# Performance work log

Hardware: AMD Instinct MI355X
Metric: run time of the kernel (lower is better)

The kernel has to match this reference:

```python
import jax, jax.numpy as jnp
import numpy as np

V = 2_000_000
NNZ = 14_000_000
N_MESHES = 4


def setup_inputs() -> dict:
    key = jax.random.key(0)
    k1, k2, k3, k4, k5, k6 = jax.random.split(key, 6)
    verts = jax.random.normal(k1, (V, 3), dtype=jnp.float32)
    lap_vals = jax.random.normal(k2, (NNZ,), dtype=jnp.float32)
    lap_rows = jax.random.randint(k3, (NNZ,), 0, V, dtype=jnp.int32)
    lap_cols = jax.random.randint(k4, (NNZ,), 0, V, dtype=jnp.int32)
    verts_mesh_idx = jnp.sort(jax.random.randint(k5, (V,), 0, N_MESHES, dtype=jnp.int32))
    coefs = jax.random.uniform(k6, (V,), dtype=jnp.float32)
    return {"verts": verts, "lap_vals": lap_vals, "lap_rows": lap_rows,
            "lap_cols": lap_cols, "verts_mesh_idx": verts_mesh_idx, "coefs": coefs}


def reference(verts, lap_vals, lap_rows, lap_cols, verts_mesh_idx, coefs):
    # Sparse Laplacian (COO) x vertex coords: L.mm(verts_packed)  [V,3]
    Lx = jax.ops.segment_sum(lap_vals[:, None] * verts[lap_cols], lap_rows,
                             num_segments=V)
    # norm_w = 1/rowsum where rowsum > 0, else unchanged (torch.sparse.sum dim=1)
    row_sum = jax.ops.segment_sum(lap_vals, lap_rows, num_segments=V)
    norm_w = jnp.where(row_sum > 0, 1.0 / jnp.where(row_sum > 0, row_sum, 1.0),
                       row_sum)[:, None]
    # 'cot' branch: loss = L.mm(verts) * norm_w - verts, then per-row L2 norm
    res = Lx * norm_w - verts
    loss = jnp.sqrt(jnp.sum(res * res, axis=1))  # [V]
    # weights = 1 / num_verts_per_mesh gathered per packed vertex
    nvpm = jnp.bincount(verts_mesh_idx, length=N_MESHES)
    weights = 1.0 / nvpm[verts_mesh_idx].astype(jnp.float32)
    loss = loss * weights * coefs
    return jnp.sum(loss) / N_MESHES
```

## Files before the change

### kernel.cpp

```cpp
#include <hip/hip_runtime.h>


#define NB 1024
#define BMAX 2048
#define BROWS 2048

__global__ void hist_kernel(const int* __restrict__ rows, int nnz, int cpb,
                            int B, unsigned short* __restrict__ hist,
                            const float* __restrict__ verts, int V,
                            float4* __restrict__ verts4) {
    if (verts4) {
        int stride = gridDim.x * blockDim.x;
        for (int vtx = blockIdx.x * blockDim.x + threadIdx.x; vtx < V;
             vtx += stride) {
            verts4[vtx] = make_float4(verts[3 * vtx + 0], verts[3 * vtx + 1],
                                      verts[3 * vtx + 2], 0.f);
        }
    }
    __shared__ unsigned h[BMAX];
    for (int b = threadIdx.x; b < B; b += blockDim.x) h[b] = 0;
    __syncthreads();
    int k = blockIdx.x;
    int i0 = k * cpb;
    int i1 = min(i0 + cpb, nnz);
    for (int i = i0 + 4 * (int)threadIdx.x; i < i1; i += 4 * blockDim.x) {
        if (i + 3 < i1) {
            int4 r4 = *(const int4*)(rows + i);
            atomicAdd(&h[r4.x >> 11], 1u);
            atomicAdd(&h[r4.y >> 11], 1u);
            atomicAdd(&h[r4.z >> 11], 1u);
            atomicAdd(&h[r4.w >> 11], 1u);
        } else {
            for (int j = i; j < i1; ++j) atomicAdd(&h[rows[j] >> 11], 1u);
        }
    }
    __syncthreads();
    for (int b = threadIdx.x; b < B; b += blockDim.x)
        hist[(size_t)b * NB + k] = (unsigned short)h[b];
}

__global__ void scan_blocks_kernel(unsigned short* __restrict__ hist,
                                   unsigned* __restrict__ total) {
    int b = blockIdx.x;
    int t = threadIdx.x;
    int lane = t & 63, wave = t >> 6;
    unsigned short* hp = hist + (size_t)b * NB;
    ushort4 hv = ((const ushort4*)hp)[t];
    unsigned a0 = hv.x, a1 = hv.y, a2 = hv.z, a3 = hv.w;
    unsigned sum = a0 + a1 + a2 + a3;
    unsigned x = sum;
    for (int off = 1; off < 64; off <<= 1) {
        unsigned y = __shfl_up(x, off);
        if (lane >= off) x += y;
    }
    __shared__ unsigned wsum[4];
    if (lane == 63) wsum[wave] = x;
    __syncthreads();
    unsigned woff = 0;
    for (int w = 0; w < wave; ++w) woff += wsum[w];
    unsigned excl = woff + x - sum;
    ushort4 ov;
    ov.x = (unsigned short)excl;
    ov.y = (unsigned short)(excl + a0);
    ov.z = (unsigned short)(excl + a0 + a1);
    ov.w = (unsigned short)(excl + a0 + a1 + a2);
    ((ushort4*)hp)[t] = ov;
    if (t == 255) total[b] = woff + x;
}

__global__ void scan_buckets_kernel(const unsigned* __restrict__ total,
                                    unsigned* __restrict__ base, int B,
                                    const int* __restrict__ mesh_idx, int v,
                                    int* __restrict__ nvpm) {
    int t = threadIdx.x;
    if (t < 4) {
        auto lb = [&](int tgt) {
            int lo = 0, hi = v;
            while (lo < hi) {
                int mid = (lo + hi) >> 1;
                if (mesh_idx[mid] < tgt) lo = mid + 1; else hi = mid;
            }
            return lo;
        };
        nvpm[t] = lb(t + 1) - lb(t);
    }
    __shared__ unsigned buf0[1024], buf1[1024];
    unsigned x0 = (2 * t < B) ? total[2 * t] : 0u;
    unsigned x1 = (2 * t + 1 < B) ? total[2 * t + 1] : 0u;
    unsigned pair = x0 + x1;
    buf0[t] = pair;
    __syncthreads();
    unsigned* src = buf0;
    unsigned* dst = buf1;
    unsigned vv = pair;
    for (int off = 1; off < 1024; off <<= 1) {
        vv = src[t];
        if (t >= off) vv += src[t - off];
        dst[t] = vv;
        __syncthreads();
        unsigned* tmp = src; src = dst; dst = tmp;
    }
    unsigned excl = vv - pair;
    base[2 * t] = excl;
    base[2 * t + 1] = excl + x0;
    if (t == 1023) base[2048] = vv;
}

__global__ void scatter_kernel(const int* __restrict__ rows,
                               const int* __restrict__ cols,
                               const float* __restrict__ vals,
                               const unsigned short* __restrict__ hist,
                               const unsigned* __restrict__ base,
                               uint2* __restrict__ dst,
                               int nnz, int cpb, int B) {
    __shared__ unsigned cur[BMAX];
    int k = blockIdx.x;
    for (int b = threadIdx.x; b < B; b += blockDim.x)
        cur[b] = base[b] + hist[(size_t)b * NB + k];
    __syncthreads();
    int i0 = k * cpb;
    int i1 = min(i0 + cpb, nnz);
    for (int i = i0 + 4 * (int)threadIdx.x; i < i1; i += 4 * blockDim.x) {
        if (i + 3 < i1) {
            int4   r4 = *(const int4*)(rows + i);
            int4   c4 = *(const int4*)(cols + i);
            float4 v4 = *(const float4*)(vals + i);
            unsigned p0 = atomicAdd(&cur[r4.x >> 11], 1u);
            unsigned p1 = atomicAdd(&cur[r4.y >> 11], 1u);
            unsigned p2 = atomicAdd(&cur[r4.z >> 11], 1u);
            unsigned p3 = atomicAdd(&cur[r4.w >> 11], 1u);
            uint2 e0, e1, e2, e3;
            e0.x = ((unsigned)(r4.x & (BROWS - 1)) << 21) | (unsigned)c4.x;
            e0.y = __float_as_uint(v4.x);
            e1.x = ((unsigned)(r4.y & (BROWS - 1)) << 21) | (unsigned)c4.y;
            e1.y = __float_as_uint(v4.y);
            e2.x = ((unsigned)(r4.z & (BROWS - 1)) << 21) | (unsigned)c4.z;
            e2.y = __float_as_uint(v4.z);
            e3.x = ((unsigned)(r4.w & (BROWS - 1)) << 21) | (unsigned)c4.w;
            e3.y = __float_as_uint(v4.w);
            dst[p0] = e0;
            dst[p1] = e1;
            dst[p2] = e2;
            dst[p3] = e3;
        } else {
            for (int j = i; j < i1; ++j) {
                int r = rows[j];
                unsigned p = atomicAdd(&cur[r >> 11], 1u);
                uint2 e;
                e.x = ((unsigned)(r & (BROWS - 1)) << 21) | (unsigned)cols[j];
                e.y = __float_as_uint(vals[j]);
                dst[p] = e;
            }
        }
    }
}

template <bool V4>
__global__ void bucket_kernel(const uint2* __restrict__ entries,
                              const unsigned* __restrict__ base,
                              const float* __restrict__ verts,
                              const float4* __restrict__ verts4,
                              const float* __restrict__ coefs,
                              const int* __restrict__ mesh_idx,
                              const int* __restrict__ nvpm,
                              double* __restrict__ partial, int V) {
    __shared__ float ax[BROWS], ay[BROWS], az[BROWS], aw[BROWS];
    int b = blockIdx.x;
    for (int j = threadIdx.x; j < BROWS; j += blockDim.x) {
        ax[j] = 0.f; ay[j] = 0.f; az[j] = 0.f; aw[j] = 0.f;
    }
    __syncthreads();
    unsigned s0 = base[b], s1 = base[b + 1];

    auto accum = [&](unsigned ex, unsigned ey) {
        unsigned lr = ex >> 21;
        unsigned c = ex & 0x1FFFFFu;
        float v = __uint_as_float(ey);
        float x, y, z;
        if (V4) {
            float4 p = verts4[c];
            x = p.x; y = p.y; z = p.z;
        } else {
            x = verts[3 * c + 0];
            y = verts[3 * c + 1];
            z = verts[3 * c + 2];
        }
        atomicAdd(&ax[lr], v * x);
        atomicAdd(&ay[lr], v * y);
        atomicAdd(&az[lr], v * z);
        atomicAdd(&aw[lr], v);
    };

    unsigned sA = s0 + (s0 & 1u);
    if (threadIdx.x == 0 && (s0 & 1u) && s0 < s1) {
        uint2 e = entries[s0];
        accum(e.x, e.y);
    }
    for (unsigned i = sA + 2 * threadIdx.x; i + 1 < s1; i += 2 * blockDim.x) {
        uint4 e = *(const uint4*)(entries + i);
        accum(e.x, e.y);
        accum(e.z, e.w);
    }
    if (threadIdx.x == 1 && s1 > sA && ((s1 - sA) & 1u)) {
        uint2 e = entries[s1 - 1];
        accum(e.x, e.y);
    }
    __syncthreads();

    float inv0 = 1.0f / (float)nvpm[0];
    float inv1 = 1.0f / (float)nvpm[1];
    float inv2 = 1.0f / (float)nvpm[2];
    float inv3 = 1.0f / (float)nvpm[3];

    double acc = 0.0;
    int r0 = b << 11;
    for (int j = threadIdx.x; j < BROWS; j += blockDim.x) {
        int r = r0 + j;
        if (r < V) {
            float rs = aw[j];
            float nw = (rs > 0.0f) ? (1.0f / rs) : rs;
            float vx, vy, vz;
            if (V4) {
                float4 p = verts4[r];
                vx = p.x; vy = p.y; vz = p.z;
            } else {
                vx = verts[3 * r + 0];
                vy = verts[3 * r + 1];
                vz = verts[3 * r + 2];
            }
            float d0 = ax[j] * nw - vx;
            float d1 = ay[j] * nw - vy;
            float d2 = az[j] * nw - vz;
            float loss = sqrtf(d0 * d0 + d1 * d1 + d2 * d2);
            int m = mesh_idx[r];
            float w = (m == 0) ? inv0 : (m == 1) ? inv1 : (m == 2) ? inv2 : inv3;
            acc += (double)(loss * w * coefs[r]);
        }
    }

    __shared__ double sred[512];
    sred[threadIdx.x] = acc;
    __syncthreads();
    for (int s = blockDim.x / 2; s > 0; s >>= 1) {
        if (threadIdx.x < s) sred[threadIdx.x] += sred[threadIdx.x + s];
        __syncthreads();
    }
    if (threadIdx.x == 0) atomicAdd(partial, sred[0]);
}

__global__ void write_out_kernel(const double* __restrict__ partial,
                                 float* __restrict__ out) {
    if (threadIdx.x == 0 && blockIdx.x == 0)
        out[0] = (float)(partial[0] * 0.25);
}


__global__ void fb_mesh_counts_kernel(const int* __restrict__ mesh_idx, int v,
                                      int* __restrict__ nvpm) {
    int m = threadIdx.x;
    if (m >= 4) return;
    auto lb = [&](int t) {
        int lo = 0, hi = v;
        while (lo < hi) {
            int mid = (lo + hi) >> 1;
            if (mesh_idx[mid] < t) lo = mid + 1; else hi = mid;
        }
        return lo;
    };
    nvpm[m] = lb(m + 1) - lb(m);
}

__global__ void fb_scatter_kernel(const float* __restrict__ verts,
                                  const float* __restrict__ vals,
                                  const int* __restrict__ rows,
                                  const int* __restrict__ cols,
                                  float* __restrict__ acc, int nnz) {
    int i = blockIdx.x * blockDim.x + threadIdx.x;
    if (i >= nnz) return;
    int r = rows[i];
    int c = cols[i];
    float v = vals[i];
    float* p = acc + 4ll * r;
    atomicAdd(p + 0, v * verts[3 * c + 0]);
    atomicAdd(p + 1, v * verts[3 * c + 1]);
    atomicAdd(p + 2, v * verts[3 * c + 2]);
    atomicAdd(p + 3, v);
}

__global__ void fb_finalize_kernel(const float* __restrict__ verts,
                                   const float* __restrict__ coefs,
                                   const int* __restrict__ mesh_idx,
                                   const float4* __restrict__ acc,
                                   const int* __restrict__ nvpm,
                                   double* __restrict__ partial, int v) {
    float inv0 = 1.0f / (float)nvpm[0];
    float inv1 = 1.0f / (float)nvpm[1];
    float inv2 = 1.0f / (float)nvpm[2];
    float inv3 = 1.0f / (float)nvpm[3];
    double acc_sum = 0.0;
    for (int i = blockIdx.x * blockDim.x + threadIdx.x; i < v;
         i += gridDim.x * blockDim.x) {
        float4 a = acc[i];
        float rs = a.w;
        float nw = (rs > 0.0f) ? (1.0f / rs) : rs;
        float r0 = a.x * nw - verts[3 * i + 0];
        float r1 = a.y * nw - verts[3 * i + 1];
        float r2 = a.z * nw - verts[3 * i + 2];
        float loss = sqrtf(r0 * r0 + r1 * r1 + r2 * r2);
        int m = mesh_idx[i];
        float w = (m == 0) ? inv0 : (m == 1) ? inv1 : (m == 2) ? inv2 : inv3;
        acc_sum += (double)(loss * w * coefs[i]);
    }
    __shared__ double sred[256];
    sred[threadIdx.x] = acc_sum;
    __syncthreads();
    for (int s = blockDim.x / 2; s > 0; s >>= 1) {
        if (threadIdx.x < s) sred[threadIdx.x] += sred[threadIdx.x + s];
        __syncthreads();
    }
    if (threadIdx.x == 0) atomicAdd(partial, sred[0]);
}

extern "C" void kernel_launch(void* const* d_in, const int* in_sizes, int n_in,
                              void* d_out, int out_size, void* d_ws, size_t ws_size,
                              hipStream_t stream) {
    const float* verts    = (const float*)d_in[0];
    const float* lap_vals = (const float*)d_in[1];
    const int*   lap_rows = (const int*)d_in[2];
    const int*   lap_cols = (const int*)d_in[3];
    const int*   mesh_idx = (const int*)d_in[4];
    const float* coefs    = (const float*)d_in[5];
    float* out = (float*)d_out;

    const int V   = in_sizes[0] / 3;
    const int NNZ = in_sizes[1];
    const int B   = (V + BROWS - 1) / BROWS;
    int cpb = (NNZ + NB - 1) / NB;
    cpb = (cpb + 3) & ~3;

    char* ws = (char*)d_ws;
    double*         partial = (double*)(ws + 0);
    int*            nvpm    = (int*)(ws + 8);
    unsigned*       base    = (unsigned*)(ws + 64);
    unsigned*       total   = (unsigned*)(ws + 16384);
    unsigned short* hist    = (unsigned short*)(ws + 32768);
    uint2*          entries = (uint2*)(ws + 32768 + (size_t)BMAX * NB * 2);

    size_t sort_need = 32768 + (size_t)BMAX * NB * 2 + (size_t)NNZ * 8 + 64;
    size_t v4_off    = (32768 + (size_t)BMAX * NB * 2 + (size_t)NNZ * 8 + 15)
                       & ~(size_t)15;
    size_t v4_need   = v4_off + (size_t)16 * V + 64;
    float4* verts4   = (float4*)(ws + v4_off);

    (void)hipMemsetAsync(d_ws, 0, 64, stream);

    if (ws_size >= sort_need && B <= BMAX && V <= (1 << 21)) {
        bool v4 = ws_size >= v4_need;
        hist_kernel<<<NB, 256, 0, stream>>>(lap_rows, NNZ, cpb, B, hist,
                                            verts, V, v4 ? verts4 : nullptr);
        scan_blocks_kernel<<<B, 256, 0, stream>>>(hist, total);
        scan_buckets_kernel<<<1, 1024, 0, stream>>>(total, base, B,
                                                    mesh_idx, V, nvpm);
        scatter_kernel<<<NB, 256, 0, stream>>>(lap_rows, lap_cols, lap_vals,
                                               hist, base, entries, NNZ, cpb, B);
        if (v4)
            bucket_kernel<true><<<B, 512, 0, stream>>>(
                entries, base, verts, verts4, coefs, mesh_idx, nvpm, partial, V);
        else
            bucket_kernel<false><<<B, 512, 0, stream>>>(
                entries, base, verts, verts4, coefs, mesh_idx, nvpm, partial, V);
    } else {
        float* acc = (float*)(ws + 64);
        (void)hipMemsetAsync(ws + 64, 0, (size_t)16 * V, stream);
        fb_mesh_counts_kernel<<<1, 64, 0, stream>>>(mesh_idx, V, nvpm);
        fb_scatter_kernel<<<(NNZ + 255) / 256, 256, 0, stream>>>(
            verts, lap_vals, lap_rows, lap_cols, acc, NNZ);
        fb_finalize_kernel<<<2048, 256, 0, stream>>>(
            verts, coefs, mesh_idx, (const float4*)acc, nvpm, partial, V);
    }

    write_out_kernel<<<1, 64, 0, stream>>>(partial, out);
}
```

Baseline: 692.5 us.

## Re-sort bucket entries by column segment to localize vertex gathers

Adds a resort pass that reorders each row bucket's entries by column segment (128K-vertex ranges) into a second entries buffer. A new bucket kernel then walks the segments in order, so concurrent blocks tend to gather verts4 from similar address ranges and get better cache locality. The price is an extra read and write of all NNZ entries, one more kernel launch, and extra workspace. It also uses nontemporal loads for the streamed entries, mesh_idx and coefs.

```diff
diff --git a/kernel.cpp b/kernel.cpp
--- a/kernel.cpp
+++ b/kernel.cpp
@@ -4,6 +4,11 @@
 #define NB 1024
 #define BMAX 2048
 #define BROWS 2048
+#define SEG_SHIFT 17
+#define NSEG_MAX 16
+
+typedef unsigned int uintv4 __attribute__((ext_vector_type(4)));
+typedef unsigned int uintv2 __attribute__((ext_vector_type(2)));
 
 __global__ void hist_kernel(const int* __restrict__ rows, int nnz, int cpb,
                             int B, unsigned short* __restrict__ hist,
@@ -155,6 +160,106 @@
     }
 }
 
+__global__ void resort_kernel(const uint2* __restrict__ src,
+                              const unsigned* __restrict__ base,
+                              uint2* __restrict__ dst,
+                              unsigned* __restrict__ segoff, int nseg) {
+    int b = blockIdx.x;
+    unsigned s0 = base[b], s1 = base[b + 1];
+    __shared__ unsigned cnt[8][NSEG_MAX];
+    __shared__ unsigned cur[NSEG_MAX];
+    int wave = threadIdx.x >> 6;
+    for (int s = threadIdx.x; s < 8 * NSEG_MAX; s += blockDim.x)
+        ((unsigned*)cnt)[s] = 0;
+    __syncthreads();
+    for (unsigned i = s0 + threadIdx.x; i < s1; i += blockDim.x) {
+        unsigned ex = ((const unsigned*)(src + i))[0];
+        atomicAdd(&cnt[wave][(ex & 0x1FFFFFu) >> SEG_SHIFT], 1u);
+    }
+    __syncthreads();
+    if (threadIdx.x == 0) {
+        unsigned acc = s0;
+        for (int s = 0; s < nseg; ++s) {
+            unsigned c = 0;
+            for (int w = 0; w < 8; ++w) c += cnt[w][s];
+            cur[s] = acc;
+            segoff[b * 17 + s] = acc;
+            acc += c;
+        }
+        segoff[b * 17 + nseg] = acc;
+    }
+    __syncthreads();
+    for (unsigned i = s0 + threadIdx.x; i < s1; i += blockDim.x) {
+        uint2 e = src[i];
+        unsigned p = atomicAdd(&cur[(e.x & 0x1FFFFFu) >> SEG_SHIFT], 1u);
+        dst[p] = e;
+    }
+}
+
+__global__ void bucket_seg_kernel(const uint2* __restrict__ entries,
+                                  const unsigned* __restrict__ segoff,
+                                  const float4* __restrict__ verts4,
+                                  const float* __restrict__ coefs,
+                                  const int* __restrict__ mesh_idx,
+                                  const int* __restrict__ nvpm,
+                                  double* __restrict__ partial, int V,
+                                  int nseg) {
+    __shared__ float ax[BROWS], ay[BROWS], az[BROWS], aw[BROWS];
+    int b = blockIdx.x;
+    for (int j = threadIdx.x; j < BROWS; j += blockDim.x) {
+        ax[j] = 0.f; ay[j] = 0.f; az[j] = 0.f; aw[j] = 0.f;
+    }
+    __syncthreads();
+    for (int s = 0; s < nseg; ++s) {
+        unsigned r0 = segoff[b * 17 + s];
+        unsigned r1 = segoff[b * 17 + s + 1];
+        for (unsigned i = r0 + threadIdx.x; i < r1; i += blockDim.x) {
+            uintv2 e = __builtin_nontemporal_load((const uintv2*)(entries + i));
+            unsigned lr = e.x >> 21;
+            unsigned c  = e.x & 0x1FFFFFu;
+            float4 p = verts4[c];
+            float v = __uint_as_float(e.y);
+            atomicAdd(&ax[lr], v * p.x);
+            atomicAdd(&ay[lr], v * p.y);
+            atomicAdd(&az[lr], v * p.z);
+            atomicAdd(&aw[lr], v);
+        }
+    }
+    __syncthreads();
+
+    float inv0 = 1.0f / (float)nvpm[0];
+    float inv1 = 1.0f / (float)nvpm[1];
+    float inv2 = 1.0f / (float)nvpm[2];
+    float inv3 = 1.0f / (float)nvpm[3];
+
+    double acc = 0.0;
+    int r0 = b << 11;
+    for (int j = threadIdx.x; j < BROWS; j += blockDim.x) {
+        int r = r0 + j;
+        if (r < V) {
+            float rs = aw[j];
+            float nw = (rs > 0.0f) ? (1.0f / rs) : rs;
+            float4 p = verts4[r];
+            float d0 = ax[j] * nw - p.x;
+            float d1 = ay[j] * nw - p.y;
+            float d2 = az[j] * nw - p.z;
+            float loss = sqrtf(d0 * d0 + d1 * d1 + d2 * d2);
+            int m = __builtin_nontemporal_load(mesh_idx + r);
+            float w = (m == 0) ? inv0 : (m == 1) ? inv1 : (m == 2) ? inv2 : inv3;
+            acc += (double)(loss * w * __builtin_nontemporal_load(coefs + r));
+        }
+    }
+
+    __shared__ double sred[512];
+    sred[threadIdx.x] = acc;
+    __syncthreads();
+    for (int s = blockDim.x / 2; s > 0; s >>= 1) {
+        if (threadIdx.x < s) sred[threadIdx.x] += sred[threadIdx.x + s];
+        __syncthreads();
+    }
+    if (threadIdx.x == 0) atomicAdd(partial, sred[0]);
+}
+
 template <bool V4>
 __global__ void bucket_kernel(const uint2* __restrict__ entries,
                               const unsigned* __restrict__ base,
@@ -172,11 +277,7 @@
     __syncthreads();
     unsigned s0 = base[b], s1 = base[b + 1];
 
-    auto accum = [&](unsigned ex, unsigned ey) {
-        unsigned lr = ex >> 21;
-        unsigned c = ex & 0x1FFFFFu;
-        float v = __uint_as_float(ey);
-        float x, y, z;
+    auto gather3 = [&](unsigned c, float& x, float& y, float& z) {
         if (V4) {
             float4 p = verts4[c];
             x = p.x; y = p.y; z = p.z;
@@ -185,25 +286,21 @@
             y = verts[3 * c + 1];
             z = verts[3 * c + 2];
         }
+    };
+    auto atomics = [&](unsigned ex, unsigned ey, float x, float y, float z) {
+        unsigned lr = ex >> 21;
+        float v = __uint_as_float(ey);
         atomicAdd(&ax[lr], v * x);
         atomicAdd(&ay[lr], v * y);
         atomicAdd(&az[lr], v * z);
         atomicAdd(&aw[lr], v);
     };
 
-    unsigned sA = s0 + (s0 & 1u);
-    if (threadIdx.x == 0 && (s0 & 1u) && s0 < s1) {
-        uint2 e = entries[s0];
-        accum(e.x, e.y);
-    }
-    for (unsigned i = sA + 2 * threadIdx.x; i + 1 < s1; i += 2 * blockDim.x) {
-        uint4 e = *(const uint4*)(entries + i);
-        accum(e.x, e.y);
-        accum(e.z, e.w);
-    }
-    if (threadIdx.x == 1 && s1 > sA && ((s1 - sA) & 1u)) {
-        uint2 e = entries[s1 - 1];
-        accum(e.x, e.y);
+    for (unsigned i = s0 + threadIdx.x; i < s1; i += blockDim.x) {
+        uint2 e = entries[i];
+        float x, y, z;
+        gather3(e.x & 0x1FFFFFu, x, y, z);
+        atomics(e.x, e.y, x, y, z);
     }
     __syncthreads();
 
@@ -220,14 +317,7 @@
             float rs = aw[j];
             float nw = (rs > 0.0f) ? (1.0f / rs) : rs;
             float vx, vy, vz;
-            if (V4) {
-                float4 p = verts4[r];
-                vx = p.x; vy = p.y; vz = p.z;
-            } else {
-                vx = verts[3 * r + 0];
-                vy = verts[3 * r + 1];
-                vz = verts[3 * r + 2];
-            }
+            gather3((unsigned)r, vx, vy, vz);
             float d0 = ax[j] * nw - vx;
             float d1 = ay[j] * nw - vy;
             float d2 = az[j] * nw - vz;
@@ -335,27 +425,34 @@
     const int V   = in_sizes[0] / 3;
     const int NNZ = in_sizes[1];
     const int B   = (V + BROWS - 1) / BROWS;
+    const int nseg = (V + (1 << SEG_SHIFT) - 1) >> SEG_SHIFT;
     int cpb = (NNZ + NB - 1) / NB;
     cpb = (cpb + 3) & ~3;
 
     char* ws = (char*)d_ws;
-    double*         partial = (double*)(ws + 0);
-    int*            nvpm    = (int*)(ws + 8);
-    unsigned*       base    = (unsigned*)(ws + 64);
-    unsigned*       total   = (unsigned*)(ws + 16384);
-    unsigned short* hist    = (unsigned short*)(ws + 32768);
-    uint2*          entries = (uint2*)(ws + 32768 + (size_t)BMAX * NB * 2);
-
-    size_t sort_need = 32768 + (size_t)BMAX * NB * 2 + (size_t)NNZ * 8 + 64;
-    size_t v4_off    = (32768 + (size_t)BMAX * NB * 2 + (size_t)NNZ * 8 + 15)
-                       & ~(size_t)15;
-    size_t v4_need   = v4_off + (size_t)16 * V + 64;
-    float4* verts4   = (float4*)(ws + v4_off);
+    const size_t off_hist     = 262144;
+    const size_t off_entries  = off_hist + (size_t)BMAX * NB * 2;
+    const size_t off_entries2 = off_entries + (size_t)NNZ * 8;
+    double*         partial  = (double*)(ws + 0);
+    int*            nvpm     = (int*)(ws + 8);
+    unsigned*       base     = (unsigned*)(ws + 64);
+    unsigned*       total    = (unsigned*)(ws + 16384);
+    unsigned*       segoff   = (unsigned*)(ws + 32768);
+    unsigned short* hist     = (unsigned short*)(ws + off_hist);
+    uint2*          entries  = (uint2*)(ws + off_entries);
+    uint2*          entries2 = (uint2*)(ws + off_entries2);
+
+    size_t sort_need = off_entries2 + 64;
+    size_t v4_need   = off_entries2 + (size_t)16 * V + 64;
+    size_t seg_need  = off_entries2 + (size_t)NNZ * 8 + (size_t)16 * V + 64;
 
     (void)hipMemsetAsync(d_ws, 0, 64, stream);
 
     if (ws_size >= sort_need && B <= BMAX && V <= (1 << 21)) {
-        bool v4 = ws_size >= v4_need;
+        bool seg = (ws_size >= seg_need) && (nseg <= NSEG_MAX);
+        bool v4  = seg || (ws_size >= v4_need);
+        float4* verts4 = seg ? (float4*)(ws + off_entries2 + (size_t)NNZ * 8)
+                             : (float4*)(ws + off_entries2);
         hist_kernel<<<NB, 256, 0, stream>>>(lap_rows, NNZ, cpb, B, hist,
                                             verts, V, v4 ? verts4 : nullptr);
         scan_blocks_kernel<<<B, 256, 0, stream>>>(hist, total);
@@ -363,12 +460,19 @@
                                                     mesh_idx, V, nvpm);
         scatter_kernel<<<NB, 256, 0, stream>>>(lap_rows, lap_cols, lap_vals,
                                                hist, base, entries, NNZ, cpb, B);
-        if (v4)
+        if (seg) {
+            resort_kernel<<<B, 512, 0, stream>>>(entries, base, entries2,
+                                                 segoff, nseg);
+            bucket_seg_kernel<<<B, 512, 0, stream>>>(entries2, segoff, verts4,
+                                                     coefs, mesh_idx, nvpm,
+                                                     partial, V, nseg);
+        } else if (v4) {
             bucket_kernel<true><<<B, 512, 0, stream>>>(
                 entries, base, verts, verts4, coefs, mesh_idx, nvpm, partial, V);
-        else
+        } else {
             bucket_kernel<false><<<B, 512, 0, stream>>>(
                 entries, base, verts, verts4, coefs, mesh_idx, nvpm, partial, V);
+        }
     } else {
         float* acc = (float*)(ws + 64);
         (void)hipMemsetAsync(ws + 64, 0, (size_t)16 * V, stream);
```

New measurement: 755.7 us. 1.09x slower.

## Drop padded float4 vertex copy, gather xyz directly, use mesh boundaries

Applied to the files above, without the earlier changes.

Removes the float4 vertex repacking pass from the histogram kernel, so the bucket kernel gathers three scalar floats per column index straight from the original vertex array. It also replaces per-row mesh_idx loads with comparisons against mesh boundary indices found by binary search, and simplifies the entry loop to one uint2 per thread instead of paired uint4 loads. This saves writing and reading a 32 MB padded copy, but the random gathers now touch up to two cache lines per vertex with three separate loads instead of one 16-byte load. Workspace offsets are also rearranged.

```diff
diff --git a/kernel.cpp b/kernel.cpp
--- a/kernel.cpp
+++ b/kernel.cpp
@@ -5,18 +5,8 @@
 #define BMAX 2048
 #define BROWS 2048
 
-__global__ void hist_kernel(const int* __restrict__ rows, int nnz, int cpb,
-                            int B, unsigned short* __restrict__ hist,
-                            const float* __restrict__ verts, int V,
-                            float4* __restrict__ verts4) {
-    if (verts4) {
-        int stride = gridDim.x * blockDim.x;
-        for (int vtx = blockIdx.x * blockDim.x + threadIdx.x; vtx < V;
-             vtx += stride) {
-            verts4[vtx] = make_float4(verts[3 * vtx + 0], verts[3 * vtx + 1],
-                                      verts[3 * vtx + 2], 0.f);
-        }
-    }
+__global__ void hist_kernel(const int* __restrict__ keys, int nnz, int cpb,
+                            int B, unsigned short* __restrict__ hist) {
     __shared__ unsigned h[BMAX];
     for (int b = threadIdx.x; b < B; b += blockDim.x) h[b] = 0;
     __syncthreads();
@@ -25,13 +15,13 @@
     int i1 = min(i0 + cpb, nnz);
     for (int i = i0 + 4 * (int)threadIdx.x; i < i1; i += 4 * blockDim.x) {
         if (i + 3 < i1) {
-            int4 r4 = *(const int4*)(rows + i);
+            int4 r4 = *(const int4*)(keys + i);
             atomicAdd(&h[r4.x >> 11], 1u);
             atomicAdd(&h[r4.y >> 11], 1u);
             atomicAdd(&h[r4.z >> 11], 1u);
             atomicAdd(&h[r4.w >> 11], 1u);
         } else {
-            for (int j = i; j < i1; ++j) atomicAdd(&h[rows[j] >> 11], 1u);
+            for (int j = i; j < i1; ++j) atomicAdd(&h[keys[j] >> 11], 1u);
         }
     }
     __syncthreads();
@@ -71,7 +61,8 @@
 __global__ void scan_buckets_kernel(const unsigned* __restrict__ total,
                                     unsigned* __restrict__ base, int B,
                                     const int* __restrict__ mesh_idx, int v,
-                                    int* __restrict__ nvpm) {
+                                    int* __restrict__ nvpm,
+                                    int* __restrict__ bnd) {
     int t = threadIdx.x;
     if (t < 4) {
         auto lb = [&](int tgt) {
@@ -82,7 +73,9 @@
             }
             return lo;
         };
-        nvpm[t] = lb(t + 1) - lb(t);
+        int hi_b = lb(t + 1);
+        nvpm[t] = hi_b - lb(t);
+        bnd[t]  = hi_b;
     }
     __shared__ unsigned buf0[1024], buf1[1024];
     unsigned x0 = (2 * t < B) ? total[2 * t] : 0u;
@@ -155,13 +148,11 @@
     }
 }
 
-template <bool V4>
 __global__ void bucket_kernel(const uint2* __restrict__ entries,
                               const unsigned* __restrict__ base,
                               const float* __restrict__ verts,
-                              const float4* __restrict__ verts4,
                               const float* __restrict__ coefs,
-                              const int* __restrict__ mesh_idx,
+                              const int* __restrict__ bnd,
                               const int* __restrict__ nvpm,
                               double* __restrict__ partial, int V) {
     __shared__ float ax[BROWS], ay[BROWS], az[BROWS], aw[BROWS];
@@ -171,39 +162,18 @@
     }
     __syncthreads();
     unsigned s0 = base[b], s1 = base[b + 1];
-
-    auto accum = [&](unsigned ex, unsigned ey) {
-        unsigned lr = ex >> 21;
-        unsigned c = ex & 0x1FFFFFu;
-        float v = __uint_as_float(ey);
-        float x, y, z;
-        if (V4) {
-            float4 p = verts4[c];
-            x = p.x; y = p.y; z = p.z;
-        } else {
-            x = verts[3 * c + 0];
-            y = verts[3 * c + 1];
-            z = verts[3 * c + 2];
-        }
+    for (unsigned i = s0 + threadIdx.x; i < s1; i += blockDim.x) {
+        uint2 e = entries[i];
+        unsigned lr = e.x >> 21;
+        unsigned c  = e.x & 0x1FFFFFu;
+        float v = __uint_as_float(e.y);
+        float x = verts[3 * c + 0];
+        float y = verts[3 * c + 1];
+        float z = verts[3 * c + 2];
         atomicAdd(&ax[lr], v * x);
         atomicAdd(&ay[lr], v * y);
         atomicAdd(&az[lr], v * z);
         atomicAdd(&aw[lr], v);
-    };
-
-    unsigned sA = s0 + (s0 & 1u);
-    if (threadIdx.x == 0 && (s0 & 1u) && s0 < s1) {
-        uint2 e = entries[s0];
-        accum(e.x, e.y);
-    }
-    for (unsigned i = sA + 2 * threadIdx.x; i + 1 < s1; i += 2 * blockDim.x) {
-        uint4 e = *(const uint4*)(entries + i);
-        accum(e.x, e.y);
-        accum(e.z, e.w);
-    }
-    if (threadIdx.x == 1 && s1 > sA && ((s1 - sA) & 1u)) {
-        uint2 e = entries[s1 - 1];
-        accum(e.x, e.y);
     }
     __syncthreads();
 
@@ -211,6 +181,7 @@
     float inv1 = 1.0f / (float)nvpm[1];
     float inv2 = 1.0f / (float)nvpm[2];
     float inv3 = 1.0f / (float)nvpm[3];
+    int bd0 = bnd[0], bd1 = bnd[1], bd2 = bnd[2];
 
     double acc = 0.0;
     int r0 = b << 11;
@@ -219,21 +190,12 @@
         if (r < V) {
             float rs = aw[j];
             float nw = (rs > 0.0f) ? (1.0f / rs) : rs;
-            float vx, vy, vz;
-            if (V4) {
-                float4 p = verts4[r];
-                vx = p.x; vy = p.y; vz = p.z;
-            } else {
-                vx = verts[3 * r + 0];
-                vy = verts[3 * r + 1];
-                vz = verts[3 * r + 2];
-            }
-            float d0 = ax[j] * nw - vx;
-            float d1 = ay[j] * nw - vy;
-            float d2 = az[j] * nw - vz;
+            float d0 = ax[j] * nw - verts[3 * r + 0];
+            float d1 = ay[j] * nw - verts[3 * r + 1];
+            float d2 = az[j] * nw - verts[3 * r + 2];
             float loss = sqrtf(d0 * d0 + d1 * d1 + d2 * d2);
-            int m = mesh_idx[r];
-            float w = (m == 0) ? inv0 : (m == 1) ? inv1 : (m == 2) ? inv2 : inv3;
+            float w = (r < bd0) ? inv0 : (r < bd1) ? inv1 : (r < bd2) ? inv2
+                                                                      : inv3;
             acc += (double)(loss * w * coefs[r]);
         }
     }
@@ -339,36 +301,30 @@
     cpb = (cpb + 3) & ~3;
 
     char* ws = (char*)d_ws;
-    double*         partial = (double*)(ws + 0);
-    int*            nvpm    = (int*)(ws + 8);
-    unsigned*       base    = (unsigned*)(ws + 64);
-    unsigned*       total   = (unsigned*)(ws + 16384);
-    unsigned short* hist    = (unsigned short*)(ws + 32768);
-    uint2*          entries = (uint2*)(ws + 32768 + (size_t)BMAX * NB * 2);
-
-    size_t sort_need = 32768 + (size_t)BMAX * NB * 2 + (size_t)NNZ * 8 + 64;
-    size_t v4_off    = (32768 + (size_t)BMAX * NB * 2 + (size_t)NNZ * 8 + 15)
-                       & ~(size_t)15;
-    size_t v4_need   = v4_off + (size_t)16 * V + 64;
-    float4* verts4   = (float4*)(ws + v4_off);
+    const size_t off_hist    = 262144;
+    const size_t off_entries = off_hist + (size_t)BMAX * NB * 2;
+    double*         partial  = (double*)(ws + 0);
+    int*            nvpm     = (int*)(ws + 8);
+    int*            bnd      = (int*)(ws + 24);
+    unsigned*       base     = (unsigned*)(ws + 64);
+    unsigned*       total    = (unsigned*)(ws + 16384);
+    unsigned short* hist     = (unsigned short*)(ws + off_hist);
+    uint2*          entries  = (uint2*)(ws + off_entries);
+
+    size_t sort_need = off_entries + (size_t)NNZ * 8 + 64;
 
     (void)hipMemsetAsync(d_ws, 0, 64, stream);
 
-    if (ws_size >= sort_need && B <= BMAX && V <= (1 << 21)) {
-        bool v4 = ws_size >= v4_need;
-        hist_kernel<<<NB, 256, 0, stream>>>(lap_rows, NNZ, cpb, B, hist,
-                                            verts, V, v4 ? verts4 : nullptr);
+    bool ok_pack = (V <= (1 << 21)) && (B <= NB) && (B <= BMAX);
+    if (ws_size >= sort_need && ok_pack) {
+        hist_kernel<<<NB, 256, 0, stream>>>(lap_rows, NNZ, cpb, B, hist);
         scan_blocks_kernel<<<B, 256, 0, stream>>>(hist, total);
         scan_buckets_kernel<<<1, 1024, 0, stream>>>(total, base, B,
-                                                    mesh_idx, V, nvpm);
-        scatter_kernel<<<NB, 256, 0, stream>>>(lap_rows, lap_cols, lap_vals,
-                                               hist, base, entries, NNZ, cpb, B);
-        if (v4)
-            bucket_kernel<true><<<B, 512, 0, stream>>>(
-                entries, base, verts, verts4, coefs, mesh_idx, nvpm, partial, V);
-        else
-            bucket_kernel<false><<<B, 512, 0, stream>>>(
-                entries, base, verts, verts4, coefs, mesh_idx, nvpm, partial, V);
+                                                    mesh_idx, V, nvpm, bnd);
+        scatter_kernel<<<NB, 256, 0, stream>>>(
+            lap_rows, lap_cols, lap_vals, hist, base, entries, NNZ, cpb, B);
+        bucket_kernel<<<B, 512, 0, stream>>>(entries, base, verts, coefs,
+                                             bnd, nvpm, partial, V);
     } else {
         float* acc = (float*)(ws + 64);
         (void)hipMemsetAsync(ws + 64, 0, (size_t)16 * V, stream);
```

Result: no change. 683.0 us (-1.4%).
